# Optimization experiments

Measured on AMD Instinct MI355X. Metric: run time of the kernel, lower is better.

Reference implementation:

```python
import jax, jax.numpy as jnp
import numpy as np

B, N, F = 64, 1000, 64          # graphs, nodes/graph, node features
E = 32000                        # edges (shared gene network)
INPUT_DIM = N * F                # 64000, flattened per-graph features
HID, L = 512, 128                # VAE hidden and latent dims
NEG_SLOPE = 0.01                 # torch LeakyReLU default


def setup_inputs() -> dict:
    key = jax.random.key(0)
    ks = jax.random.split(key, 16)
    s = lambda *sh: 1.0 / np.sqrt(sh[0])
    return {
        "x": jax.random.normal(ks[0], (B, N, F), jnp.float32),
        "edge_index": jax.random.randint(ks[1], (2, E), 0, N),
        "eps": jax.random.normal(ks[2], (B, L), jnp.float32),
        # GeneralConv message linear (in==out, skip is identity residual)
        "W_msg": jax.random.normal(ks[3], (F, F), jnp.float32) * s(F),
        "b_msg": jnp.zeros((F,), jnp.float32),
        # VAE encoder
        "W_e1": jax.random.normal(ks[4], (INPUT_DIM, HID), jnp.float32) * s(INPUT_DIM),
        "b_e1": jnp.zeros((HID,), jnp.float32),
        "W_mean": jax.random.normal(ks[5], (HID, L), jnp.float32) * s(HID),
        "b_mean": jnp.zeros((L,), jnp.float32),
        "W_lv": jax.random.normal(ks[6], (HID, L), jnp.float32) * s(HID),
        "b_lv": jnp.zeros((L,), jnp.float32),
        # VAE decoder
        "W_d1": jax.random.normal(ks[7], (L, HID), jnp.float32) * s(L),
        "b_d1": jnp.zeros((HID,), jnp.float32),
        "W_d2": jax.random.normal(ks[8], (HID, INPUT_DIM), jnp.float32) * s(HID),
        "b_d2": jnp.zeros((INPUT_DIM,), jnp.float32),
    }


def reference(x, edge_index, eps, W_msg, b_msg, W_e1, b_e1, W_mean, b_mean,
              W_lv, b_lv, W_d1, b_d1, W_d2, b_d2):
    src, dst = edge_index[0], edge_index[1]
    # --- GeneralConv (mean aggr, identity skip), batched over all graphs ---
    msg = jnp.einsum('bef,fg->beg', x[:, src, :], W_msg) + b_msg   # [B,E,F]
    agg = jnp.zeros_like(x).at[:, dst, :].add(msg)                  # scatter-sum
    deg = jnp.zeros((N,), x.dtype).at[dst].add(1.0)
    agg = agg / jnp.maximum(deg, 1.0)[None, :, None]                # mean
    h = agg + x                                                     # skip connection
    h = jnp.where(h >= 0, h, NEG_SLOPE * h)                         # LeakyReLU
    # dropout(p=0.1) is identity in eval mode
    xs = h.reshape(B, INPUT_DIM)
    # --- VAE ---
    he = jax.nn.relu(xs @ W_e1 + b_e1)
    mean = he @ W_mean + b_mean
    log_var = he @ W_lv + b_lv
    z = mean + jnp.exp(0.5 * log_var) * eps                         # reparameterize
    hd = jax.nn.relu(z @ W_d1 + b_d1)
    x_hat = jax.nn.sigmoid(hd @ W_d2 + b_d2)
    return x_hat, mean, log_var
```

## Files before the change

kernel.cpp:

```cpp
#include <hip/hip_runtime.h>
#include <cstdint>
#include <cstddef>

constexpr int kB   = 64;
constexpr int kN   = 1000;
constexpr int kF   = 64;
constexpr int kE   = 32000;
constexpr int kIn  = 64000;
constexpr int kHid = 512;
constexpr int kLat = 128;
constexpr float kSlope = 0.01f;

constexpr int KC  = 256;
constexpr int NKC = kIn / KC;

constexpr size_t OFF_OFFS   = 0;
constexpr size_t OFF_DEGF   = 4096;
constexpr size_t OFF_INVD   = 8192;
constexpr size_t OFF_BUCKET = 12288;
constexpr size_t OFF_XS     = 140288;
constexpr size_t OFF_HE     = OFF_XS  + (size_t)kB * kIn  * 4;
constexpr size_t OFF_HDT    = OFF_HE  + (size_t)kB * kHid * 4;
constexpr size_t OFF_PART   = OFF_HDT + (size_t)kHid * kB * 4;
constexpr size_t WS_NEED    = OFF_PART + (size_t)NKC * kB * kHid * 4;

__global__ __launch_bounds__(1024) void gnn_k_pre(
    const int* __restrict__ ei, int* __restrict__ offs, int* __restrict__ bucket,
    float* __restrict__ degf, float* __restrict__ invd) {
    __shared__ int s_deg[kN];
    __shared__ int s_scan[1024];
    __shared__ int s_cur[kN];
    int t = threadIdx.x;
    if (t < kN) s_deg[t] = 0;
    __syncthreads();
    for (int e = t; e < kE; e += 1024) atomicAdd(&s_deg[ei[kE + e]], 1);
    __syncthreads();
    int v = (t < kN) ? s_deg[t] : 0;
    s_scan[t] = v;
    __syncthreads();
    for (int d = 1; d < 1024; d <<= 1) {
        int add = (t >= d) ? s_scan[t - d] : 0;
        __syncthreads();
        s_scan[t] += add;
        __syncthreads();
    }
    if (t < kN) {
        int excl = s_scan[t] - v;
        offs[t]  = excl;
        s_cur[t] = excl;
        degf[t]  = (float)v;
        invd[t]  = 1.0f / fmaxf((float)v, 1.0f);
    }
    if (t == kN - 1) offs[kN] = s_scan[t];
    __syncthreads();
    for (int e = t; e < kE; e += 1024) {
        int d = ei[kE + e];
        int pos = atomicAdd(&s_cur[d], 1);
        bucket[pos] = ei[e];
    }
}

__global__ __launch_bounds__(256) void gnn_k_conv(
    const float* __restrict__ x, const float* __restrict__ Wm,
    const float* __restrict__ bm, const int* __restrict__ offs,
    const int* __restrict__ bucket, const float* __restrict__ degf,
    const float* __restrict__ invd, float* __restrict__ xs) {
    int blk  = blockIdx.x;
    int b    = blk / (kN / 4);
    int ng   = blk - b * (kN / 4);
    int wave = threadIdx.x >> 6;
    int f    = threadIdx.x & 63;
    int n    = ng * 4 + wave;
    const float* xb = x + (size_t)b * kIn;
    int beg = offs[n], end = offs[n + 1];
    float a0 = 0.f, a1 = 0.f;
    int i = beg;
    for (; i + 2 <= end; i += 2) {
        int s0 = bucket[i], s1 = bucket[i + 1];
        a0 += xb[s0 * kF + f];
        a1 += xb[s1 * kF + f];
    }
    if (i < end) a0 += xb[bucket[i] * kF + f];
    float acc = a0 + a1;
    float d0 = 0.f, d1 = 0.f, d2 = 0.f, d3 = 0.f;
    #pragma unroll
    for (int ff = 0; ff < kF; ff += 4) {
        d0 = fmaf(__shfl(acc, ff    ), Wm[(ff    ) * kF + f], d0);
        d1 = fmaf(__shfl(acc, ff + 1), Wm[(ff + 1) * kF + f], d1);
        d2 = fmaf(__shfl(acc, ff + 2), Wm[(ff + 2) * kF + f], d2);
        d3 = fmaf(__shfl(acc, ff + 3), Wm[(ff + 3) * kF + f], d3);
    }
    float dot = (d0 + d1) + (d2 + d3);
    float dg  = degf[n];
    float val = (dot + dg * bm[f]) * invd[n];
    float hv  = val + xb[n * kF + f];
    hv = hv >= 0.f ? hv : kSlope * hv;
    xs[(size_t)b * kIn + n * kF + f] = hv;
}

template <bool ATOMIC>
__global__ __launch_bounds__(256) void gnn_k_enc(
    const float* __restrict__ xs, const float* __restrict__ We1,
    float* __restrict__ out) {
    int c  = blockIdx.x;
    int by = blockIdx.y;
    int t  = threadIdx.x;
    int nl = t & 63;
    int mg = t >> 6;
    int k0 = c * KC;
    int cb = by * 256 + nl * 4;
    int m0 = mg * 16;

    __shared__ float s_x[kB][KC];
    const float4* xs4 = (const float4*)xs;
    #pragma unroll
    for (int i = t; i < kB * (KC / 4); i += 256) {
        int m  = i >> 6;
        int jw = i & 63;
        *(float4*)&s_x[m][jw * 4] = xs4[(size_t)m * (kIn / 4) + (k0 >> 2) + jw];
    }
    __syncthreads();

    float acc[16][4];
    #pragma unroll
    for (int mm = 0; mm < 16; ++mm)
        #pragma unroll
        for (int j = 0; j < 4; ++j) acc[mm][j] = 0.f;

    const float* wbase = We1 + (size_t)k0 * kHid + cb;
    for (int kk = 0; kk < KC; kk += 4) {
        const float* wk = wbase + (size_t)kk * kHid;
        float4 w0 = *(const float4*)(wk);
        float4 w1 = *(const float4*)(wk + kHid);
        float4 w2 = *(const float4*)(wk + 2 * kHid);
        float4 w3 = *(const float4*)(wk + 3 * kHid);
        #pragma unroll
        for (int mm = 0; mm < 16; ++mm) {
            float4 xv = *(const float4*)&s_x[m0 + mm][kk];
            acc[mm][0] = fmaf(xv.x, w0.x, fmaf(xv.y, w1.x, fmaf(xv.z, w2.x, fmaf(xv.w, w3.x, acc[mm][0]))));
            acc[mm][1] = fmaf(xv.x, w0.y, fmaf(xv.y, w1.y, fmaf(xv.z, w2.y, fmaf(xv.w, w3.y, acc[mm][1]))));
            acc[mm][2] = fmaf(xv.x, w0.z, fmaf(xv.y, w1.z, fmaf(xv.z, w2.z, fmaf(xv.w, w3.z, acc[mm][2]))));
            acc[mm][3] = fmaf(xv.x, w0.w, fmaf(xv.y, w1.w, fmaf(xv.z, w2.w, fmaf(xv.w, w3.w, acc[mm][3]))));
        }
    }

    if (ATOMIC) {
        #pragma unroll
        for (int mm = 0; mm < 16; ++mm)
            #pragma unroll
            for (int j = 0; j < 4; ++j)
                atomicAdd(&out[(size_t)(m0 + mm) * kHid + cb + j], acc[mm][j]);
    } else {
        #pragma unroll
        for (int mm = 0; mm < 16; ++mm) {
            float4 v = make_float4(acc[mm][0], acc[mm][1], acc[mm][2], acc[mm][3]);
            *(float4*)&out[((size_t)c * kB + m0 + mm) * kHid + cb] = v;
        }
    }
}

__global__ __launch_bounds__(256) void gnn_k_encred(
    const float* __restrict__ part, const float* __restrict__ be1,
    float* __restrict__ he) {
    int id = blockIdx.x * 256 + threadIdx.x;
    int n = id & 511, m = id >> 9;
    float s0 = 0.f, s1 = 0.f, s2 = 0.f, s3 = 0.f;
    const float* p = part + (size_t)m * kHid + n;
    #pragma unroll 2
    for (int c = 0; c < NKC; c += 4) {
        s0 += p[(size_t)(c    ) * kB * kHid];
        s1 += p[(size_t)(c + 1) * kB * kHid];
        s2 += p[(size_t)(c + 2) * kB * kHid];
        s3 += p[(size_t)(c + 3) * kB * kHid];
    }
    float s = (s0 + s1) + (s2 + s3) + be1[n];
    he[id] = fmaxf(s, 0.f);
}

__global__ void gnn_k_hefin(float* __restrict__ he, const float* __restrict__ be1) {
    int i = blockIdx.x * 256 + threadIdx.x;
    if (i < kB * kHid) {
        float v = he[i] + be1[i & 511];
        he[i] = v > 0.f ? v : 0.f;
    }
}

__global__ __launch_bounds__(512) void gnn_k_latdec1(
    const float* __restrict__ he, const float* __restrict__ Wmean,
    const float* __restrict__ bmean, const float* __restrict__ Wlv,
    const float* __restrict__ blv, const float* __restrict__ eps,
    const float* __restrict__ Wd1, const float* __restrict__ bd1,
    float* __restrict__ outMean, float* __restrict__ outLv,
    float* __restrict__ hdT) {
    int b = blockIdx.x;
    int t = threadIdx.x;
    __shared__ float s_he[kHid];
    __shared__ float s_z[kLat];
    s_he[t] = he[(size_t)b * kHid + t];
    __syncthreads();
    if (t < kLat) {
        float dm = bmean[t], dv = blv[t];
        float dm1 = 0.f, dv1 = 0.f;
        #pragma unroll 4
        for (int k = 0; k < kHid; k += 2) {
            float h0 = s_he[k], h1 = s_he[k + 1];
            dm  = fmaf(h0, Wmean[(size_t)k * kLat + t], dm);
            dm1 = fmaf(h1, Wmean[(size_t)(k + 1) * kLat + t], dm1);
            dv  = fmaf(h0, Wlv[(size_t)k * kLat + t], dv);
            dv1 = fmaf(h1, Wlv[(size_t)(k + 1) * kLat + t], dv1);
        }
        dm += dm1; dv += dv1;
        outMean[b * kLat + t] = dm;
        outLv[b * kLat + t]   = dv;
        s_z[t] = fmaf(expf(0.5f * dv), eps[b * kLat + t], dm);
    }
    __syncthreads();
    float acc = bd1[t];
    float acc1 = 0.f;
    #pragma unroll 4
    for (int k = 0; k < kLat; k += 2) {
        acc  = fmaf(s_z[k],     Wd1[(size_t)k * kHid + t], acc);
        acc1 = fmaf(s_z[k + 1], Wd1[(size_t)(k + 1) * kHid + t], acc1);
    }
    acc += acc1;
    hdT[(size_t)t * kB + b] = fmaxf(acc, 0.f);
}

constexpr int DKC = 128;
__global__ __launch_bounds__(512) void gnn_k_dec2(
    const float* __restrict__ hdT, const float* __restrict__ Wd2,
    const float* __restrict__ bd2, float* __restrict__ out) {
    int t  = threadIdx.x;
    int ng = t & 31;
    int mg = t >> 5;
    int n0 = blockIdx.x * 128 + ng * 4;
    int m0 = mg * 4;

    __shared__ float s_hd[DKC][kB];

    float acc[4][4];
    #pragma unroll
    for (int i = 0; i < 4; ++i)
        #pragma unroll
        for (int j = 0; j < 4; ++j) acc[i][j] = 0.f;

    for (int kc = 0; kc < kHid; kc += DKC) {
        const float4* src = (const float4*)(hdT + (size_t)kc * kB);
        float4* dst = (float4*)&s_hd[0][0];
        #pragma unroll
        for (int r = 0; r < 4; ++r) dst[t + 512 * r] = src[t + 512 * r];
        __syncthreads();

        const float* wp = Wd2 + (size_t)kc * kIn + n0;
        #pragma unroll 4
        for (int k = 0; k < DKC; ++k) {
            float4 w = *(const float4*)(wp + (size_t)k * kIn);
            float4 h = *(const float4*)&s_hd[k][m0];
            acc[0][0] = fmaf(h.x, w.x, acc[0][0]);
            acc[0][1] = fmaf(h.x, w.y, acc[0][1]);
            acc[0][2] = fmaf(h.x, w.z, acc[0][2]);
            acc[0][3] = fmaf(h.x, w.w, acc[0][3]);
            acc[1][0] = fmaf(h.y, w.x, acc[1][0]);
            acc[1][1] = fmaf(h.y, w.y, acc[1][1]);
            acc[1][2] = fmaf(h.y, w.z, acc[1][2]);
            acc[1][3] = fmaf(h.y, w.w, acc[1][3]);
            acc[2][0] = fmaf(h.z, w.x, acc[2][0]);
            acc[2][1] = fmaf(h.z, w.y, acc[2][1]);
            acc[2][2] = fmaf(h.z, w.z, acc[2][2]);
            acc[2][3] = fmaf(h.z, w.w, acc[2][3]);
            acc[3][0] = fmaf(h.w, w.x, acc[3][0]);
            acc[3][1] = fmaf(h.w, w.y, acc[3][1]);
            acc[3][2] = fmaf(h.w, w.z, acc[3][2]);
            acc[3][3] = fmaf(h.w, w.w, acc[3][3]);
        }
        __syncthreads();
    }

    float4 bb = *(const float4*)(bd2 + n0);
    #pragma unroll
    for (int i = 0; i < 4; ++i) {
        float4 v;
        v.x = 1.f / (1.f + expf(-(acc[i][0] + bb.x)));
        v.y = 1.f / (1.f + expf(-(acc[i][1] + bb.y)));
        v.z = 1.f / (1.f + expf(-(acc[i][2] + bb.z)));
        v.w = 1.f / (1.f + expf(-(acc[i][3] + bb.w)));
        *(float4*)(out + (size_t)(m0 + i) * kIn + n0) = v;
    }
}

extern "C" void kernel_launch(void* const* d_in, const int* in_sizes, int n_in,
                              void* d_out, int out_size, void* d_ws, size_t ws_size,
                              hipStream_t stream) {
    const float* x     = (const float*)d_in[0];
    const int*   ei    = (const int*)d_in[1];
    const float* eps   = (const float*)d_in[2];
    const float* Wm    = (const float*)d_in[3];
    const float* bm    = (const float*)d_in[4];
    const float* We1   = (const float*)d_in[5];
    const float* be1   = (const float*)d_in[6];
    const float* Wmean = (const float*)d_in[7];
    const float* bmean = (const float*)d_in[8];
    const float* Wlv   = (const float*)d_in[9];
    const float* blv   = (const float*)d_in[10];
    const float* Wd1   = (const float*)d_in[11];
    const float* bd1   = (const float*)d_in[12];
    const float* Wd2   = (const float*)d_in[13];
    const float* bd2   = (const float*)d_in[14];
    float* out = (float*)d_out;

    char* ws = (char*)d_ws;
    int*   offs   = (int*)(ws + OFF_OFFS);
    float* degf   = (float*)(ws + OFF_DEGF);
    float* invd   = (float*)(ws + OFF_INVD);
    int*   bucket = (int*)(ws + OFF_BUCKET);
    float* xs     = (float*)(ws + OFF_XS);
    float* he     = (float*)(ws + OFF_HE);
    float* hdT    = (float*)(ws + OFF_HDT);
    float* part   = (float*)(ws + OFF_PART);

    float* outMean = out + (size_t)kB * kIn;
    float* outLv   = outMean + (size_t)kB * kLat;

    gnn_k_pre<<<1, 1024, 0, stream>>>(ei, offs, bucket, degf, invd);
    gnn_k_conv<<<kB * (kN / 4), 256, 0, stream>>>(x, Wm, bm, offs, bucket, degf, invd, xs);

    if (ws_size >= WS_NEED) {
        gnn_k_enc<false><<<dim3(NKC, 2), 256, 0, stream>>>(xs, We1, part);
        gnn_k_encred<<<kB * kHid / 256, 256, 0, stream>>>(part, be1, he);
    } else {
        hipMemsetAsync(he, 0, (size_t)kB * kHid * 4, stream);
        gnn_k_enc<true><<<dim3(NKC, 2), 256, 0, stream>>>(xs, We1, he);
        gnn_k_hefin<<<(kB * kHid + 255) / 256, 256, 0, stream>>>(he, be1);
    }

    gnn_k_latdec1<<<kB, kHid, 0, stream>>>(he, Wmean, bmean, Wlv, blv, eps,
                                           Wd1, bd1, outMean, outLv, hdT);
    gnn_k_dec2<<<kIn / 128, 512, 0, stream>>>(hdT, Wd2, bd2, out);
}
```

Measured before the change: 624.6 us.

## Process two graphs per conv block, widen encoder blocks, fuse split-K reduce into latent kernel

```diff
diff --git a/kernel.cpp b/kernel.cpp
--- a/kernel.cpp
+++ b/kernel.cpp
@@ -65,41 +65,68 @@
     const float* __restrict__ bm, const int* __restrict__ offs,
     const int* __restrict__ bucket, const float* __restrict__ degf,
     const float* __restrict__ invd, float* __restrict__ xs) {
-    int blk  = blockIdx.x;
-    int b    = blk / (kN / 4);
-    int ng   = blk - b * (kN / 4);
+    int bid = blockIdx.x;
+    int wg  = (bid & 7) * 1000 + (bid >> 3);
+    int bp  = wg / (kN / 4);
+    int ng  = wg - bp * (kN / 4);
     int wave = threadIdx.x >> 6;
     int f    = threadIdx.x & 63;
     int n    = ng * 4 + wave;
-    const float* xb = x + (size_t)b * kIn;
+    int b0   = bp * 2;
+    const float* xb0 = x + (size_t)b0 * kIn;
+    const float* xb1 = xb0 + kIn;
     int beg = offs[n], end = offs[n + 1];
-    float a0 = 0.f, a1 = 0.f;
+    float p0 = 0.f, p1 = 0.f, q0 = 0.f, q1 = 0.f;
+    float r0 = 0.f, r1 = 0.f, u0 = 0.f, u1 = 0.f;
     int i = beg;
-    for (; i + 2 <= end; i += 2) {
-        int s0 = bucket[i], s1 = bucket[i + 1];
-        a0 += xb[s0 * kF + f];
-        a1 += xb[s1 * kF + f];
-    }
-    if (i < end) a0 += xb[bucket[i] * kF + f];
-    float acc = a0 + a1;
-    float d0 = 0.f, d1 = 0.f, d2 = 0.f, d3 = 0.f;
+    for (; i + 4 <= end; i += 4) {
+        int i0 = bucket[i]     * kF + f;
+        int i1 = bucket[i + 1] * kF + f;
+        int i2 = bucket[i + 2] * kF + f;
+        int i3 = bucket[i + 3] * kF + f;
+        p0 += xb0[i0]; p1 += xb1[i0];
+        q0 += xb0[i1]; q1 += xb1[i1];
+        r0 += xb0[i2]; r1 += xb1[i2];
+        u0 += xb0[i3]; u1 += xb1[i3];
+    }
+    for (; i < end; ++i) {
+        int i0 = bucket[i] * kF + f;
+        p0 += xb0[i0]; p1 += xb1[i0];
+    }
+    float acc0 = (p0 + q0) + (r0 + u0);
+    float acc1 = (p1 + q1) + (r1 + u1);
+    float d00 = 0.f, d01 = 0.f, d02 = 0.f, d03 = 0.f;
+    float d10 = 0.f, d11 = 0.f, d12 = 0.f, d13 = 0.f;
     #pragma unroll
     for (int ff = 0; ff < kF; ff += 4) {
-        d0 = fmaf(__shfl(acc, ff    ), Wm[(ff    ) * kF + f], d0);
-        d1 = fmaf(__shfl(acc, ff + 1), Wm[(ff + 1) * kF + f], d1);
-        d2 = fmaf(__shfl(acc, ff + 2), Wm[(ff + 2) * kF + f], d2);
-        d3 = fmaf(__shfl(acc, ff + 3), Wm[(ff + 3) * kF + f], d3);
-    }
-    float dot = (d0 + d1) + (d2 + d3);
+        float w0 = Wm[(ff    ) * kF + f];
+        float w1 = Wm[(ff + 1) * kF + f];
+        float w2 = Wm[(ff + 2) * kF + f];
+        float w3 = Wm[(ff + 3) * kF + f];
+        d00 = fmaf(__shfl(acc0, ff    ), w0, d00);
+        d01 = fmaf(__shfl(acc0, ff + 1), w1, d01);
+        d02 = fmaf(__shfl(acc0, ff + 2), w2, d02);
+        d03 = fmaf(__shfl(acc0, ff + 3), w3, d03);
+        d10 = fmaf(__shfl(acc1, ff    ), w0, d10);
+        d11 = fmaf(__shfl(acc1, ff + 1), w1, d11);
+        d12 = fmaf(__shfl(acc1, ff + 2), w2, d12);
+        d13 = fmaf(__shfl(acc1, ff + 3), w3, d13);
+    }
+    float dot0 = (d00 + d01) + (d02 + d03);
+    float dot1 = (d10 + d11) + (d12 + d13);
     float dg  = degf[n];
-    float val = (dot + dg * bm[f]) * invd[n];
-    float hv  = val + xb[n * kF + f];
-    hv = hv >= 0.f ? hv : kSlope * hv;
-    xs[(size_t)b * kIn + n * kF + f] = hv;
+    float iv  = invd[n];
+    float bmf = bm[f];
+    float v0 = (dot0 + dg * bmf) * iv + xb0[n * kF + f];
+    float v1 = (dot1 + dg * bmf) * iv + xb1[n * kF + f];
+    v0 = v0 >= 0.f ? v0 : kSlope * v0;
+    v1 = v1 >= 0.f ? v1 : kSlope * v1;
+    xs[(size_t)b0 * kIn + n * kF + f] = v0;
+    xs[(size_t)(b0 + 1) * kIn + n * kF + f] = v1;
 }
 
 template <bool ATOMIC>
-__global__ __launch_bounds__(256) void gnn_k_enc(
+__global__ __launch_bounds__(512) void gnn_k_enc(
     const float* __restrict__ xs, const float* __restrict__ We1,
     float* __restrict__ out) {
     int c  = blockIdx.x;
@@ -109,21 +136,21 @@
     int mg = t >> 6;
     int k0 = c * KC;
     int cb = by * 256 + nl * 4;
-    int m0 = mg * 16;
+    int m0 = mg * 8;
 
     __shared__ float s_x[kB][KC];
     const float4* xs4 = (const float4*)xs;
     #pragma unroll
-    for (int i = t; i < kB * (KC / 4); i += 256) {
+    for (int i = t; i < kB * (KC / 4); i += 512) {
         int m  = i >> 6;
         int jw = i & 63;
         *(float4*)&s_x[m][jw * 4] = xs4[(size_t)m * (kIn / 4) + (k0 >> 2) + jw];
     }
     __syncthreads();
 
-    float acc[16][4];
-    #pragma unroll
-    for (int mm = 0; mm < 16; ++mm)
+    float acc[8][4];
+    #pragma unroll
+    for (int mm = 0; mm < 8; ++mm)
         #pragma unroll
         for (int j = 0; j < 4; ++j) acc[mm][j] = 0.f;
 
@@ -135,7 +162,7 @@
         float4 w2 = *(const float4*)(wk + 2 * kHid);
         float4 w3 = *(const float4*)(wk + 3 * kHid);
         #pragma unroll
-        for (int mm = 0; mm < 16; ++mm) {
+        for (int mm = 0; mm < 8; ++mm) {
             float4 xv = *(const float4*)&s_x[m0 + mm][kk];
             acc[mm][0] = fmaf(xv.x, w0.x, fmaf(xv.y, w1.x, fmaf(xv.z, w2.x, fmaf(xv.w, w3.x, acc[mm][0]))));
             acc[mm][1] = fmaf(xv.x, w0.y, fmaf(xv.y, w1.y, fmaf(xv.z, w2.y, fmaf(xv.w, w3.y, acc[mm][1]))));
@@ -146,35 +173,17 @@
 
     if (ATOMIC) {
         #pragma unroll
-        for (int mm = 0; mm < 16; ++mm)
+        for (int mm = 0; mm < 8; ++mm)
             #pragma unroll
             for (int j = 0; j < 4; ++j)
                 atomicAdd(&out[(size_t)(m0 + mm) * kHid + cb + j], acc[mm][j]);
     } else {
         #pragma unroll
-        for (int mm = 0; mm < 16; ++mm) {
+        for (int mm = 0; mm < 8; ++mm) {
             float4 v = make_float4(acc[mm][0], acc[mm][1], acc[mm][2], acc[mm][3]);
             *(float4*)&out[((size_t)c * kB + m0 + mm) * kHid + cb] = v;
         }
     }
-}
-
-__global__ __launch_bounds__(256) void gnn_k_encred(
-    const float* __restrict__ part, const float* __restrict__ be1,
-    float* __restrict__ he) {
-    int id = blockIdx.x * 256 + threadIdx.x;
-    int n = id & 511, m = id >> 9;
-    float s0 = 0.f, s1 = 0.f, s2 = 0.f, s3 = 0.f;
-    const float* p = part + (size_t)m * kHid + n;
-    #pragma unroll 2
-    for (int c = 0; c < NKC; c += 4) {
-        s0 += p[(size_t)(c    ) * kB * kHid];
-        s1 += p[(size_t)(c + 1) * kB * kHid];
-        s2 += p[(size_t)(c + 2) * kB * kHid];
-        s3 += p[(size_t)(c + 3) * kB * kHid];
-    }
-    float s = (s0 + s1) + (s2 + s3) + be1[n];
-    he[id] = fmaxf(s, 0.f);
 }
 
 __global__ void gnn_k_hefin(float* __restrict__ he, const float* __restrict__ be1) {
@@ -185,10 +194,12 @@
     }
 }
 
+template <bool RED>
 __global__ __launch_bounds__(512) void gnn_k_latdec1(
-    const float* __restrict__ he, const float* __restrict__ Wmean,
-    const float* __restrict__ bmean, const float* __restrict__ Wlv,
-    const float* __restrict__ blv, const float* __restrict__ eps,
+    const float* __restrict__ hesrc, const float* __restrict__ be1,
+    const float* __restrict__ Wmean, const float* __restrict__ bmean,
+    const float* __restrict__ Wlv, const float* __restrict__ blv,
+    const float* __restrict__ eps,
     const float* __restrict__ Wd1, const float* __restrict__ bd1,
     float* __restrict__ outMean, float* __restrict__ outLv,
     float* __restrict__ hdT) {
@@ -196,7 +207,22 @@
     int t = threadIdx.x;
     __shared__ float s_he[kHid];
     __shared__ float s_z[kLat];
-    s_he[t] = he[(size_t)b * kHid + t];
+    if (RED) {
+        const float* p = hesrc + (size_t)b * kHid + t;
+        float s0 = 0.f, s1 = 0.f, s2 = 0.f, s3 = 0.f;
+        int c = 0;
+        for (; c + 4 <= NKC; c += 4) {
+            s0 += p[(size_t)(c    ) * kB * kHid];
+            s1 += p[(size_t)(c + 1) * kB * kHid];
+            s2 += p[(size_t)(c + 2) * kB * kHid];
+            s3 += p[(size_t)(c + 3) * kB * kHid];
+        }
+        for (; c < NKC; ++c) s0 += p[(size_t)c * kB * kHid];
+        float s = (s0 + s1) + (s2 + s3) + be1[t];
+        s_he[t] = fmaxf(s, 0.f);
+    } else {
+        s_he[t] = hesrc[(size_t)b * kHid + t];
+    }
     __syncthreads();
     if (t < kLat) {
         float dm = bmean[t], dv = blv[t];
@@ -322,18 +348,22 @@
     float* outLv   = outMean + (size_t)kB * kLat;
 
     gnn_k_pre<<<1, 1024, 0, stream>>>(ei, offs, bucket, degf, invd);
-    gnn_k_conv<<<kB * (kN / 4), 256, 0, stream>>>(x, Wm, bm, offs, bucket, degf, invd, xs);
+    gnn_k_conv<<<(kB / 2) * (kN / 4), 256, 0, stream>>>(x, Wm, bm, offs, bucket,
+                                                        degf, invd, xs);
 
     if (ws_size >= WS_NEED) {
-        gnn_k_enc<false><<<dim3(NKC, 2), 256, 0, stream>>>(xs, We1, part);
-        gnn_k_encred<<<kB * kHid / 256, 256, 0, stream>>>(part, be1, he);
+        gnn_k_enc<false><<<dim3(NKC, 2), 512, 0, stream>>>(xs, We1, part);
+        gnn_k_latdec1<true><<<kB, kHid, 0, stream>>>(part, be1, Wmean, bmean, Wlv,
+                                                     blv, eps, Wd1, bd1,
+                                                     outMean, outLv, hdT);
     } else {
         hipMemsetAsync(he, 0, (size_t)kB * kHid * 4, stream);
-        gnn_k_enc<true><<<dim3(NKC, 2), 256, 0, stream>>>(xs, We1, he);
+        gnn_k_enc<true><<<dim3(NKC, 2), 512, 0, stream>>>(xs, We1, he);
         gnn_k_hefin<<<(kB * kHid + 255) / 256, 256, 0, stream>>>(he, be1);
-    }
-
-    gnn_k_latdec1<<<kB, kHid, 0, stream>>>(he, Wmean, bmean, Wlv, blv, eps,
-                                           Wd1, bd1, outMean, outLv, hdT);
+        gnn_k_latdec1<false><<<kB, kHid, 0, stream>>>(he, be1, Wmean, bmean, Wlv,
+                                                      blv, eps, Wd1, bd1,
+                                                      outMean, outLv, hdT);
+    }
+
     gnn_k_dec2<<<kIn / 128, 512, 0, stream>>>(hdT, Wd2, bd2, out);
 }
```

Measured after the change: 568.2 us. 1.1x faster.
